# Optimization experiments

Measured on AMD Instinct MI355X. Metric: run time of the kernel, lower is better.

The kernel has to match this reference:

```python
import jax, jax.numpy as jnp
import numpy as np

EPS = 1e-12  # matches torch F.normalize default eps


def setup_inputs() -> dict:
    key = jax.random.key(0)
    ks = jax.random.split(key, 8)
    B, N, D, H = 8, 2048, 128, 128
    s = 1.0 / np.sqrt(D)
    return {
        "x": jax.random.normal(ks[0], (B, N, D), dtype=jnp.float32),
        "edge_weight": jax.random.uniform(ks[1], (B, N, N), dtype=jnp.float32),
        "W0": jax.random.normal(ks[2], (D, H), dtype=jnp.float32) * s,
        "b0": jnp.zeros((H,), dtype=jnp.float32),
        "W1": jax.random.normal(ks[3], (H, H), dtype=jnp.float32) * s,
        "b1": jnp.zeros((H,), dtype=jnp.float32),
        "W2": jax.random.normal(ks[4], (H, H), dtype=jnp.float32) * s,
        "b2": jnp.zeros((H,), dtype=jnp.float32),
    }


def _adapt_conv(h, edge_weight, W, b, is_last):
    h = h @ W + b                                   # [B,N,H]
    norm = jnp.linalg.norm(h, axis=-1, keepdims=True)
    nh = h / jnp.maximum(norm, EPS)                 # L2 normalize (F.normalize)
    cos = jnp.einsum('bij,bkj->bik', nh, nh)        # [B,N,N] cosine similarity
    ew = edge_weight * cos                          # elementwise mask
    h = jnp.einsum('bpq,bqc->bpc', ew, h)           # weighted aggregation
    if not is_last:
        h = jax.nn.relu(h)                          # dropout p=0.0 -> identity
    return h


def reference(x, edge_weight, W0, b0, W1, b1, W2, b2):
    params = [(W0, b0), (W1, b1), (W2, b2)]
    h = x
    n_layers = len(params)
    for i, (W, b) in enumerate(params):
        h = _adapt_conv(h, edge_weight, W, b, is_last=(i == n_layers - 1))
    return h
```

## Files before the change

kernel.cpp:

```cpp
#include <hip/hip_runtime.h>
#include <hip/hip_bf16.h>
#include <math.h>


typedef __attribute__((ext_vector_type(8)))  short bf16x8;
typedef __attribute__((ext_vector_type(4)))  short bf16x4;
typedef __attribute__((ext_vector_type(4)))  float f32x4;
typedef __attribute__((ext_vector_type(16))) float f32x16;
typedef __attribute__((ext_vector_type(2)))  unsigned u32x2;

static constexpr int kB = 8, kN = 2048, kH = 128;

static __device__ __forceinline__ ushort bf16bits(float f) {
    __hip_bfloat16 hb = __float2bfloat16(f);
    return *reinterpret_cast<ushort*>(&hb);
}
static __device__ __forceinline__ unsigned pk2(float lo, float hi) {
    return (unsigned)bf16bits(lo) | ((unsigned)bf16bits(hi) << 16);
}
static __device__ __forceinline__ float bf2f_lo(unsigned u) {
    unsigned v = u << 16; float f; __builtin_memcpy(&f, &v, 4); return f;
}
static __device__ __forceinline__ float bf2f_hi(unsigned u) {
    unsigned v = u & 0xffff0000u; float f; __builtin_memcpy(&f, &v, 4); return f;
}

#define LDS_BARRIER()                                          \
    do {                                                       \
        asm volatile("s_waitcnt lgkmcnt(0)" ::: "memory");     \
        __builtin_amdgcn_s_barrier();                          \
        __builtin_amdgcn_sched_barrier(0);                     \
    } while (0)

__global__ __launch_bounds__(256) void cvt_bf16_kernel(
    const float* __restrict__ src, ushort* __restrict__ dst, int n4)
{
    int i = blockIdx.x * 256 + threadIdx.x;
    if (i >= n4) return;
    float4 v = ((const float4*)src)[i];
    bf16x4 o;
    o[0] = (short)bf16bits(v.x); o[1] = (short)bf16bits(v.y);
    o[2] = (short)bf16bits(v.z); o[3] = (short)bf16bits(v.w);
    ((bf16x4*)dst)[i] = o;
}

__global__ __launch_bounds__(256) void cvt_wT_kernel(
    const float* __restrict__ W0, const float* __restrict__ W1,
    const float* __restrict__ W2, ushort* __restrict__ WT)
{
    const float* W = blockIdx.y == 0 ? W0 : (blockIdx.y == 1 ? W1 : W2);
    int i = blockIdx.x * 256 + threadIdx.x;
    int d = i >> 7, c = i & 127;
    WT[(size_t)blockIdx.y * kH * kH + c * kH + d] = bf16bits(W[d * kH + c]);
}

__global__ __launch_bounds__(256) void linear_tr_kernel(
    const ushort* __restrict__ h16, const ushort* __restrict__ WT,
    const float* __restrict__ bias, ushort* __restrict__ tn16,
    ushort* __restrict__ tT16)
{
    __shared__ float ssb[64][2];
    __shared__ ushort tr[128 * 72];
    __shared__ ushort trn[64 * 136];

    const int tid = threadIdx.x, lane = tid & 63, wid = tid >> 6;
    const int wr = wid >> 1, wc = wid & 1, quad = lane >> 4, l16 = lane & 15;
    const int rowbase = blockIdx.x * 64;
    const int b = rowbase / kN, q0 = rowbase % kN;

    f32x4 acc[2][4];
#pragma unroll
    for (int i = 0; i < 2; ++i)
#pragma unroll
        for (int ct = 0; ct < 4; ++ct) acc[i][ct] = (f32x4){0.f, 0.f, 0.f, 0.f};

#pragma unroll
    for (int k = 0; k < 4; ++k) {
        bf16x8 Af[2], Bf[4];
#pragma unroll
        for (int i = 0; i < 2; ++i)
            Af[i] = *(const bf16x8*)&h16[(size_t)(rowbase + wr * 32 + i * 16 + l16) * kH + k * 32 + quad * 8];
#pragma unroll
        for (int ct = 0; ct < 4; ++ct)
            Bf[ct] = *(const bf16x8*)&WT[(size_t)(wc * 64 + ct * 16 + l16) * kH + k * 32 + quad * 8];
#pragma unroll
        for (int i = 0; i < 2; ++i)
#pragma unroll
            for (int ct = 0; ct < 4; ++ct)
                acc[i][ct] = __builtin_amdgcn_mfma_f32_16x16x32_bf16(Af[i], Bf[ct], acc[i][ct], 0, 0, 0);
    }

    float bsr[4];
#pragma unroll
    for (int ct = 0; ct < 4; ++ct) bsr[ct] = bias[wc * 64 + ct * 16 + l16];

    f32x4 ss[2] = {(f32x4){0,0,0,0}, (f32x4){0,0,0,0}};
#pragma unroll
    for (int i = 0; i < 2; ++i)
#pragma unroll
        for (int ct = 0; ct < 4; ++ct)
#pragma unroll
            for (int r = 0; r < 4; ++r) {
                float v = acc[i][ct][r] + bsr[ct];
                acc[i][ct][r] = v;
                ss[i][r] += v * v;
            }
#pragma unroll
    for (int step = 1; step < 16; step <<= 1)
#pragma unroll
        for (int i = 0; i < 2; ++i)
#pragma unroll
            for (int r = 0; r < 4; ++r) ss[i][r] += __shfl_xor(ss[i][r], step);

    if (l16 == 0)
#pragma unroll
        for (int i = 0; i < 2; ++i)
#pragma unroll
            for (int r = 0; r < 4; ++r)
                ssb[wr * 32 + i * 16 + quad * 4 + r][wc] = ss[i][r];
    __syncthreads();

    float invr[2][4];
#pragma unroll
    for (int i = 0; i < 2; ++i)
#pragma unroll
        for (int r = 0; r < 4; ++r) {
            const int pl = wr * 32 + i * 16 + quad * 4 + r;
            float s2 = ssb[pl][0] + ssb[pl][1];
            invr[i][r] = 1.f / fmaxf(sqrtf(s2), 1e-12f);
        }

#pragma unroll
    for (int i = 0; i < 2; ++i)
#pragma unroll
        for (int ct = 0; ct < 4; ++ct)
#pragma unroll
            for (int r = 0; r < 4; ++r) {
                const int pl = wr * 32 + i * 16 + quad * 4 + r;
                const int c = wc * 64 + ct * 16 + l16;
                const float v = acc[i][ct][r];
                tr[c * 72 + pl] = bf16bits(v);
                trn[pl * 136 + c] = bf16bits(v * invr[i][r]);
            }
    __syncthreads();

    ushort* tTb = tT16 + (size_t)b * kH * kN;
#pragma unroll
    for (int it = 0; it < 4; ++it) {
        int idx = tid + 256 * it;
        int c = idx >> 3, ch = idx & 7;
        bf16x8 v = *(const bf16x8*)&tr[c * 72 + ch * 8];
        *(bf16x8*)&tTb[(size_t)c * kN + q0 + ch * 8] = v;
    }
#pragma unroll
    for (int it = 0; it < 4; ++it) {
        int idx = tid + 256 * it;
        int p = idx >> 4, ch = idx & 15;
        bf16x8 v = *(const bf16x8*)&trn[p * 136 + ch * 8];
        *(bf16x8*)&tn16[(size_t)(rowbase + p) * kH + ch * 8] = v;
    }
}

__global__ __launch_bounds__(256, 2) void agg_kernel(
    const ushort* __restrict__ tn, const ushort* __restrict__ tT,
    const float* __restrict__ ew,
    ushort* __restrict__ hout, float* __restrict__ fout, int last)
{
    __shared__ char lds[73728];

    const int b = blockIdx.x, pbase = blockIdx.y * 32;
    const int tid = threadIdx.x, lane = tid & 63, wq = tid >> 6;
    const int l31 = lane & 31, h = lane >> 5;

    const ushort* tb  = tn + (size_t)b * kN * kH;
    const ushort* tTb = tT + (size_t)b * kH * kN;
    const float*  ewb = ew + (size_t)b * kN * kN;

    char* TQ   = lds;
    char* TT   = lds + 32768;
    char* myEw = lds + 65536 + wq * 2048;

    bf16x8 tP[8];
#pragma unroll
    for (int m = 0; m < 8; ++m)
        tP[m] = *(const bf16x8*)&tb[(size_t)(pbase + l31) * kH + m * 16 + h * 8];

    f32x16 oacc[4];
#pragma unroll
    for (int ct = 0; ct < 4; ++ct)
#pragma unroll
        for (int r = 0; r < 16; ++r) oacc[ct][r] = 0.f;

    const int sgRow = tid >> 4, sgCh = tid & 15;
    const int ewR = lane >> 3, ewQ = lane & 7;

    bf16x8 rQ[8], rT[8];
    f32x4 eC[4];

    auto prefetch = [&](int qb) {
#pragma unroll
        for (int j = 0; j < 8; ++j) {
            rQ[j] = *(const bf16x8*)&tb[(size_t)(qb + sgRow + 16 * j) * kH + sgCh * 8];
            rT[j] = *(const bf16x8*)&tTb[(size_t)(sgRow + 16 * j) * kN + qb + sgCh * 8];
        }
#pragma unroll
        for (int j = 0; j < 4; ++j)
            eC[j] = *(const f32x4*)&ewb[(size_t)(pbase + 8 * j + ewR) * kN + qb + wq * 32 + ewQ * 4];
    };
    prefetch(0);

    auto buildFrags = [&](const f32x16& sa, const f32x16& sb, bf16x8* out2) {
        float sv[16];
#pragma unroll
        for (int g = 0; g < 4; ++g) {
            u32x2 ev = *(const u32x2*)&myEw[l31 * 64 + ((16 * g + 8 * h) ^ ((l31 & 7) << 3))];
            sv[4 * g + 0] = (sa[4 * g + 0] + sb[4 * g + 0]) * bf2f_lo(ev[0]);
            sv[4 * g + 1] = (sa[4 * g + 1] + sb[4 * g + 1]) * bf2f_hi(ev[0]);
            sv[4 * g + 2] = (sa[4 * g + 2] + sb[4 * g + 2]) * bf2f_lo(ev[1]);
            sv[4 * g + 3] = (sa[4 * g + 3] + sb[4 * g + 3]) * bf2f_hi(ev[1]);
        }
#pragma unroll
        for (int kk = 0; kk < 2; ++kk) {
            const int e0 = kk * 8;
            unsigned a0 = pk2(sv[e0 + 0], sv[e0 + 1]);
            unsigned a1 = pk2(sv[e0 + 2], sv[e0 + 3]);
            unsigned b0 = pk2(sv[e0 + 4], sv[e0 + 5]);
            unsigned b1 = pk2(sv[e0 + 6], sv[e0 + 7]);
            asm("v_permlane32_swap_b32 %0, %1" : "+v"(a0), "+v"(b0));
            asm("v_permlane32_swap_b32 %0, %1" : "+v"(a1), "+v"(b1));
            union { unsigned u[4]; bf16x8 v; } U;
            U.u[0] = a0;
            U.u[1] = a1;
            U.u[2] = b0;
            U.u[3] = b1;
            out2[kk] = U.v;
        }
    };

    for (int it = 0; it < 16; ++it) {
        const int qb = it * 128;

#pragma unroll
        for (int j = 0; j < 8; ++j) {
            const int row = sgRow + 16 * j;
            const int swz = (row & 15) << 4;
            *(bf16x8*)&TQ[row * 256 + ((sgCh * 16) ^ swz)] = rQ[j];
            *(bf16x8*)&TT[row * 256 + ((sgCh * 16) ^ swz)] = rT[j];
        }
#pragma unroll
        for (int j = 0; j < 4; ++j) {
            const int row = 8 * j + ewR;
            u32x2 w;
            w[0] = pk2(eC[j][0], eC[j][1]);
            w[1] = pk2(eC[j][2], eC[j][3]);
            *(u32x2*)&myEw[row * 64 + ((ewQ * 8) ^ ((row & 7) << 3))] = w;
        }

        if (it < 15) prefetch(qb + 128);

        LDS_BARRIER();

        f32x16 s0a, s0b;
#pragma unroll
        for (int r = 0; r < 16; ++r) { s0a[r] = 0.f; s0b[r] = 0.f; }
        const int qrow = wq * 32 + l31;
        const int qswz = (qrow & 15) << 4;
#pragma unroll
        for (int m = 0; m < 8; ++m) {
            bf16x8 a = *(const bf16x8*)&TQ[qrow * 256 + ((m * 32 + 16 * h) ^ qswz)];
            if (m & 1) s0b = __builtin_amdgcn_mfma_f32_32x32x16_bf16(a, tP[m], s0b, 0, 0, 0);
            else       s0a = __builtin_amdgcn_mfma_f32_32x32x16_bf16(a, tP[m], s0a, 0, 0, 0);
        }

        bf16x8 aw[2];
        buildFrags(s0a, s0b, aw);

#pragma unroll
        for (int kkt = 0; kkt < 2; ++kkt) {
#pragma unroll
            for (int ct = 0; ct < 4; ++ct) {
                const int crow = 32 * ct + l31;
                bf16x8 Bf = *(const bf16x8*)&TT[crow * 256 +
                              ((wq * 64 + kkt * 32 + 16 * h) ^ ((crow & 15) << 4))];
                oacc[ct] = __builtin_amdgcn_mfma_f32_32x32x16_bf16(aw[kkt], Bf, oacc[ct], 0, 0, 0);
            }
        }
        LDS_BARRIER();
    }

    float* OL = (float*)lds;
#pragma unroll
    for (int w = 0; w < 4; ++w) {
        if (wq == w) {
#pragma unroll
            for (int ct = 0; ct < 4; ++ct)
#pragma unroll
                for (int r = 0; r < 16; ++r) {
                    const int pl = (r & 3) + 8 * (r >> 2) + 4 * h;
                    const int idx = pl * 128 + 32 * ct + l31;
                    if (w == 0) OL[idx] = oacc[ct][r];
                    else        OL[idx] += oacc[ct][r];
                }
        }
        __syncthreads();
    }

    {
        const int p = tid >> 3, cb = (tid & 7) * 16;
        const size_t gbase = (size_t)b * kN * kH + (size_t)(pbase + p) * kH + cb;
        if (!last) {
#pragma unroll
            for (int u = 0; u < 2; ++u) {
                bf16x8 o;
#pragma unroll
                for (int k = 0; k < 8; ++k)
                    o[k] = (short)bf16bits(fmaxf(OL[p * 128 + cb + u * 8 + k], 0.f));
                *(bf16x8*)&hout[gbase + u * 8] = o;
            }
        } else {
#pragma unroll
            for (int u = 0; u < 4; ++u) {
                f32x4 o;
#pragma unroll
                for (int k = 0; k < 4; ++k)
                    o[k] = OL[p * 128 + cb + u * 4 + k];
                *(f32x4*)&fout[gbase + u * 4] = o;
            }
        }
    }
}

extern "C" void kernel_launch(void* const* d_in, const int* in_sizes, int n_in,
                              void* d_out, int out_size, void* d_ws, size_t ws_size,
                              hipStream_t stream) {
    const float* x  = (const float*)d_in[0];
    const float* ew = (const float*)d_in[1];
    const float* W0 = (const float*)d_in[2];
    const float* b0 = (const float*)d_in[3];
    const float* W1 = (const float*)d_in[4];
    const float* b1 = (const float*)d_in[5];
    const float* W2 = (const float*)d_in[6];
    const float* b2 = (const float*)d_in[7];
    const float* bias[3] = {b0, b1, b2};

    const size_t nBNH = (size_t)kB * kN * kH;
    ushort* h16  = (ushort*)d_ws;
    ushort* tn16 = h16 + nBNH;
    ushort* tT16 = tn16 + nBNH;
    ushort* WT   = tT16 + nBNH;
    float*  out  = (float*)d_out;

    cvt_bf16_kernel<<<(int)(nBNH / 4 + 255) / 256, 256, 0, stream>>>(x, h16, (int)(nBNH / 4));
    cvt_wT_kernel<<<dim3(64, 3), 256, 0, stream>>>(W0, W1, W2, WT);

    for (int layer = 0; layer < 3; ++layer) {
        linear_tr_kernel<<<kB * kN / 64, 256, 0, stream>>>(
            h16, WT + (size_t)layer * kH * kH, bias[layer], tn16, tT16);
        agg_kernel<<<dim3(kB, kN / 32), 256, 0, stream>>>(
            tn16, tT16, ew, h16, out, layer == 2 ? 1 : 0);
    }
}
```

Measured before the change: 353.7 us.

## Double-buffer agg tiles via direct global-to-LDS loads with 64-row blocks

The aggregation kernel now uses 512-thread blocks covering 64 output rows instead of 32. Two row groups share each staged Q/T tile, which halves per-row tile traffic. Tiles are loaded straight into double-buffered LDS with global_load_lds, so the next tile streams in during the current MFMA work and the register staging and copy pass are gone. In exchange, LDS use grows to about 144KB per block, allowing only one block per CU. Correctness also depends on the barrier draining the async LDS loads.

```diff
diff --git a/kernel.cpp b/kernel.cpp
--- a/kernel.cpp
+++ b/kernel.cpp
@@ -25,12 +25,11 @@
     unsigned v = u & 0xffff0000u; float f; __builtin_memcpy(&f, &v, 4); return f;
 }
 
-#define LDS_BARRIER()                                          \
-    do {                                                       \
-        asm volatile("s_waitcnt lgkmcnt(0)" ::: "memory");     \
-        __builtin_amdgcn_s_barrier();                          \
-        __builtin_amdgcn_sched_barrier(0);                     \
-    } while (0)
+typedef __attribute__((address_space(1))) const unsigned gu32;
+typedef __attribute__((address_space(3))) unsigned lu32;
+static __device__ __forceinline__ void gload16(const void* g, void* l) {
+    __builtin_amdgcn_global_load_lds((gu32*)g, (lu32*)l, 16, 0, 0);
+}
 
 __global__ __launch_bounds__(256) void cvt_bf16_kernel(
     const float* __restrict__ src, ushort* __restrict__ dst, int n4)
@@ -161,29 +160,31 @@
     }
 }
 
-__global__ __launch_bounds__(256, 2) void agg_kernel(
+__global__ __launch_bounds__(512, 2) void agg_kernel(
     const ushort* __restrict__ tn, const ushort* __restrict__ tT,
     const float* __restrict__ ew,
     ushort* __restrict__ hout, float* __restrict__ fout, int last)
 {
-    __shared__ char lds[73728];
-
-    const int b = blockIdx.x, pbase = blockIdx.y * 32;
-    const int tid = threadIdx.x, lane = tid & 63, wq = tid >> 6;
+    __shared__ char TQs[2][32768];
+    __shared__ char TTs[2][32768];
+    __shared__ char ews[8][2048];
+
+    const int b = blockIdx.x, pbase = blockIdx.y * 64;
+    const int tid = threadIdx.x, lane = tid & 63, wid = tid >> 6;
+    const int wp = wid >> 2, wq = wid & 3;
     const int l31 = lane & 31, h = lane >> 5;
 
     const ushort* tb  = tn + (size_t)b * kN * kH;
     const ushort* tTb = tT + (size_t)b * kH * kN;
     const float*  ewb = ew + (size_t)b * kN * kN;
 
-    char* TQ   = lds;
-    char* TT   = lds + 32768;
-    char* myEw = lds + 65536 + wq * 2048;
+    char* myEw = &ews[wid][0];
+    const int pbg = pbase + wp * 32;
 
     bf16x8 tP[8];
 #pragma unroll
     for (int m = 0; m < 8; ++m)
-        tP[m] = *(const bf16x8*)&tb[(size_t)(pbase + l31) * kH + m * 16 + h * 8];
+        tP[m] = *(const bf16x8*)&tb[(size_t)(pbg + l31) * kH + m * 16 + h * 8];
 
     f32x16 oacc[4];
 #pragma unroll
@@ -191,23 +192,29 @@
 #pragma unroll
         for (int r = 0; r < 16; ++r) oacc[ct][r] = 0.f;
 
-    const int sgRow = tid >> 4, sgCh = tid & 15;
+    const int dRow = lane >> 4, dCh = lane & 15;
     const int ewR = lane >> 3, ewQ = lane & 7;
 
-    bf16x8 rQ[8], rT[8];
     f32x4 eC[4];
 
-    auto prefetch = [&](int qb) {
-#pragma unroll
-        for (int j = 0; j < 8; ++j) {
-            rQ[j] = *(const bf16x8*)&tb[(size_t)(qb + sgRow + 16 * j) * kH + sgCh * 8];
-            rT[j] = *(const bf16x8*)&tTb[(size_t)(sgRow + 16 * j) * kN + qb + sgCh * 8];
-        }
+    auto issueTile = [&](int qb, int buf) {
+#pragma unroll
+        for (int p = 0; p < 4; ++p) {
+            const int r0 = wid * 16 + p * 4;
+            const int row = r0 + dRow;
+            gload16(&tb [(size_t)(qb + row) * kH + ((dCh ^ (row & 15)) * 8)], &TQs[buf][r0 * 256]);
+            gload16(&tTb[(size_t)row * kN + qb + ((dCh ^ (row & 15)) * 8)],  &TTs[buf][r0 * 256]);
+        }
+    };
+    auto loadEw = [&](int qb) {
 #pragma unroll
         for (int j = 0; j < 4; ++j)
-            eC[j] = *(const f32x4*)&ewb[(size_t)(pbase + 8 * j + ewR) * kN + qb + wq * 32 + ewQ * 4];
+            eC[j] = *(const f32x4*)&ewb[(size_t)(pbg + 8 * j + ewR) * kN + qb + wq * 32 + ewQ * 4];
     };
-    prefetch(0);
+
+    issueTile(0, 0);
+    loadEw(0);
+    __syncthreads();
 
     auto buildFrags = [&](const f32x16& sa, const f32x16& sb, bf16x8* out2) {
         float sv[16];
@@ -238,15 +245,8 @@
     };
 
     for (int it = 0; it < 16; ++it) {
-        const int qb = it * 128;
-
-#pragma unroll
-        for (int j = 0; j < 8; ++j) {
-            const int row = sgRow + 16 * j;
-            const int swz = (row & 15) << 4;
-            *(bf16x8*)&TQ[row * 256 + ((sgCh * 16) ^ swz)] = rQ[j];
-            *(bf16x8*)&TT[row * 256 + ((sgCh * 16) ^ swz)] = rT[j];
-        }
+        const int buf = it & 1;
+
 #pragma unroll
         for (int j = 0; j < 4; ++j) {
             const int row = 8 * j + ewR;
@@ -256,9 +256,10 @@
             *(u32x2*)&myEw[row * 64 + ((ewQ * 8) ^ ((row & 7) << 3))] = w;
         }
 
-        if (it < 15) prefetch(qb + 128);
-
-        LDS_BARRIER();
+        if (it < 15) {
+            issueTile((it + 1) * 128, buf ^ 1);
+            loadEw((it + 1) * 128);
+        }
 
         f32x16 s0a, s0b;
 #pragma unroll
@@ -267,7 +268,7 @@
         const int qswz = (qrow & 15) << 4;
 #pragma unroll
         for (int m = 0; m < 8; ++m) {
-            bf16x8 a = *(const bf16x8*)&TQ[qrow * 256 + ((m * 32 + 16 * h) ^ qswz)];
+            bf16x8 a = *(const bf16x8*)&TQs[buf][qrow * 256 + ((m * 32 + 16 * h) ^ qswz)];
             if (m & 1) s0b = __builtin_amdgcn_mfma_f32_32x32x16_bf16(a, tP[m], s0b, 0, 0, 0);
             else       s0a = __builtin_amdgcn_mfma_f32_32x32x16_bf16(a, tP[m], s0a, 0, 0, 0);
         }
@@ -280,15 +281,16 @@
 #pragma unroll
             for (int ct = 0; ct < 4; ++ct) {
                 const int crow = 32 * ct + l31;
-                bf16x8 Bf = *(const bf16x8*)&TT[crow * 256 +
+                bf16x8 Bf = *(const bf16x8*)&TTs[buf][crow * 256 +
                               ((wq * 64 + kkt * 32 + 16 * h) ^ ((crow & 15) << 4))];
                 oacc[ct] = __builtin_amdgcn_mfma_f32_32x32x16_bf16(aw[kkt], Bf, oacc[ct], 0, 0, 0);
             }
         }
-        LDS_BARRIER();
-    }
-
-    float* OL = (float*)lds;
+
+        __syncthreads();
+    }
+
+    float* OL = (float*)&TQs[0][0];
 #pragma unroll
     for (int w = 0; w < 4; ++w) {
         if (wq == w) {
@@ -296,7 +298,7 @@
             for (int ct = 0; ct < 4; ++ct)
 #pragma unroll
                 for (int r = 0; r < 16; ++r) {
-                    const int pl = (r & 3) + 8 * (r >> 2) + 4 * h;
+                    const int pl = wp * 32 + (r & 3) + 8 * (r >> 2) + 4 * h;
                     const int idx = pl * 128 + 32 * ct + l31;
                     if (w == 0) OL[idx] = oacc[ct][r];
                     else        OL[idx] += oacc[ct][r];
@@ -356,7 +358,7 @@
     for (int layer = 0; layer < 3; ++layer) {
         linear_tr_kernel<<<kB * kN / 64, 256, 0, stream>>>(
             h16, WT + (size_t)layer * kH * kH, bias[layer], tn16, tT16);
-        agg_kernel<<<dim3(kB, kN / 32), 256, 0, stream>>>(
+        agg_kernel<<<dim3(kB, kN / 64), 512, 0, stream>>>(
             tn16, tT16, ew, h16, out, layer == 2 ? 1 : 0);
     }
 }
```

Measured after the change: 327.4 us. 7.4% less time.
